# Optimization experiments

Hardware: AMD Instinct MI355X
Metric: run time of the kernel (lower is better)

## Reference

```python
import jax, jax.numpy as jnp
import numpy as np

N_NODES = 50000
N_EDGES = 600000
N_GRAPHS = 1024
D = 128
NEG_SLOPE = 0.2


def _gat_conv(x, W, a_src, a_dst, b, src, dst, n):
    # PyG GATConv, heads=1, concat=True, add_self_loops=True (self loops
    # already appended to src/dst by the caller).
    h = x @ W                                  # [N, C]
    alpha_src = h @ a_src                      # [N]
    alpha_dst = h @ a_dst                      # [N]
    e = jax.nn.leaky_relu(alpha_src[src] + alpha_dst[dst], NEG_SLOPE)  # [E']
    # segment softmax over incoming edges of each destination node
    e_max = jax.ops.segment_max(e, dst, num_segments=n)
    ex = jnp.exp(e - e_max[dst])
    denom = jax.ops.segment_sum(ex, dst, num_segments=n)
    alpha = ex / denom[dst]
    out = jax.ops.segment_sum(h[src] * alpha[:, None], dst, num_segments=n)
    return out + b


def _global_mean_pool(x, batch, n_graphs):
    s = jax.ops.segment_sum(x, batch, num_segments=n_graphs)
    cnt = jax.ops.segment_sum(jnp.ones((x.shape[0],), x.dtype), batch,
                              num_segments=n_graphs)
    return s / jnp.maximum(cnt, 1.0)[:, None]


def setup_inputs() -> dict:
    key = jax.random.key(0)
    ks = jax.random.split(key, 12)
    x = jax.random.normal(ks[0], (N_NODES, D), dtype=jnp.float32)
    edge_index = jax.random.randint(ks[1], (2, N_EDGES), 0, N_NODES, dtype=jnp.int64)
    batch = jnp.sort(jax.random.randint(ks[2], (N_NODES,), 0, N_GRAPHS, dtype=jnp.int64))
    glorot = 1.0 / np.sqrt(D)
    return {
        "x": x,
        "edge_index": edge_index,
        "batch": batch,
        "W1": jax.random.normal(ks[3], (D, D), dtype=jnp.float32) * glorot,
        "att_src1": jax.random.normal(ks[4], (D,), dtype=jnp.float32) * glorot,
        "att_dst1": jax.random.normal(ks[5], (D,), dtype=jnp.float32) * glorot,
        "b1": jnp.zeros((D,), dtype=jnp.float32),
        "W2": jax.random.normal(ks[6], (D, D), dtype=jnp.float32) * glorot,
        "att_src2": jax.random.normal(ks[7], (D,), dtype=jnp.float32) * glorot,
        "att_dst2": jax.random.normal(ks[8], (D,), dtype=jnp.float32) * glorot,
        "b2": jnp.zeros((D,), dtype=jnp.float32),
    }


def reference(x, edge_index, batch, W1, att_src1, att_dst1, b1,
              W2, att_src2, att_dst2, b2):
    n = x.shape[0]
    loops = jnp.arange(n, dtype=edge_index.dtype)
    src = jnp.concatenate([edge_index[0], loops])
    dst = jnp.concatenate([edge_index[1], loops])

    h1 = jax.nn.relu(_gat_conv(x, W1, att_src1, att_dst1, b1, src, dst, n))
    emb1 = _global_mean_pool(h1, batch, N_GRAPHS)

    h2 = jax.nn.relu(_gat_conv(h1, W2, att_src2, att_dst2, b2, src, dst, n))
    emb2 = _global_mean_pool(h2, batch, N_GRAPHS)

    return (emb1, emb2)
```

## Files before the change

### kernel.cpp

```cpp
#include <hip/hip_runtime.h>
#include <hip/hip_fp16.h>
#include <cstdint>
#include <cstddef>

#define NN 50000
#define NE 600000
#define NT (NE + NN)
#define NG 1024
#define D 128
#define NEG_SLOPE 0.2f
#define MAXDEG 64

typedef _Float16 half8 __attribute__((ext_vector_type(8)));
typedef float f32x4 __attribute__((ext_vector_type(4)));

__global__ void prep_misc(const float* __restrict__ W1, const float* __restrict__ W2,
                          _Float16* __restrict__ Wt1, _Float16* __restrict__ Wt2,
                          const int* __restrict__ batch, int* __restrict__ gptr,
                          unsigned* __restrict__ deg) {
    int i = blockIdx.x * 256 + threadIdx.x;
    if (i < NN) deg[i] = 0u;
    if (i < 2 * D * D) {
        const float* W  = (i < D * D) ? W1 : W2;
        _Float16*   Wt  = (i < D * D) ? Wt1 : Wt2;
        int j = i & (D * D - 1);
        int k = j >> 7, c = j & 127;
        Wt[c * D + k] = (_Float16)W[j];
    }
    if (i <= NG) {
        int lo = 0, hi = NN;
        while (lo < hi) { int mid = (lo + hi) >> 1; if (batch[mid] < i) lo = mid + 1; else hi = mid; }
        gptr[i] = lo;
    }
}

__global__ void build_kernel(const int* __restrict__ ei0, const int* __restrict__ ei1,
                             unsigned* __restrict__ deg,
                             unsigned short* __restrict__ bucket) {
    int e = blockIdx.x * blockDim.x + threadIdx.x;
    if (e >= NT) return;
    int s, d;
    if (e < NE) { s = ei0[e]; d = ei1[e]; } else { s = d = e - NE; }
    unsigned pos = atomicAdd(deg + d, 1u);
    if (pos < MAXDEG) bucket[(size_t)d * MAXDEG + pos] = (unsigned short)s;
}

template <bool FP16IN>
__global__ __launch_bounds__(256) void gemm_mfma(
    const void* __restrict__ Xv, const _Float16* __restrict__ Wt,
    const float* __restrict__ a_s, const float* __restrict__ a_d,
    __half2* __restrict__ Hh, float* __restrict__ AS, float* __restrict__ AD)
{
    __shared__ _Float16 Ht[64][132];
    int t = threadIdx.x;
    int w = t >> 6, lane = t & 63;
    int rowlane = lane & 15, kg = lane >> 4;
    int rb = (int)blockIdx.x * 64;
    int r0 = rb + w * 16;
    int r  = r0 + rowlane;
    int rc = r < NN ? r : NN - 1;

    half8 afr[4];
    if constexpr (FP16IN) {
        const _Float16* xr = (const _Float16*)Xv + (size_t)rc * D + kg * 8;
        #pragma unroll
        for (int kt = 0; kt < 4; ++kt)
            afr[kt] = *reinterpret_cast<const half8*>(xr + kt * 32);
    } else {
        const float* xr = (const float*)Xv + (size_t)rc * D + kg * 8;
        #pragma unroll
        for (int kt = 0; kt < 4; ++kt) {
            float4 u = *reinterpret_cast<const float4*>(xr + kt * 32);
            float4 v = *reinterpret_cast<const float4*>(xr + kt * 32 + 4);
            half8 a;
            a[0] = (_Float16)u.x; a[1] = (_Float16)u.y;
            a[2] = (_Float16)u.z; a[3] = (_Float16)u.w;
            a[4] = (_Float16)v.x; a[5] = (_Float16)v.y;
            a[6] = (_Float16)v.z; a[7] = (_Float16)v.w;
            afr[kt] = a;
        }
    }

    f32x4 acc[8];
    #pragma unroll
    for (int i = 0; i < 8; ++i) acc[i] = (f32x4){0.f, 0.f, 0.f, 0.f};

    const _Float16* wb = Wt + (size_t)rowlane * D + kg * 8;
    #pragma unroll
    for (int ct = 0; ct < 8; ++ct) {
        const _Float16* wc = wb + (size_t)ct * 16 * D;
        #pragma unroll
        for (int kt = 0; kt < 4; ++kt) {
            half8 b = *reinterpret_cast<const half8*>(wc + kt * 32);
            acc[ct] = __builtin_amdgcn_mfma_f32_16x16x32_f16(afr[kt], b, acc[ct], 0, 0, 0);
        }
    }

    float rs[4] = {0.f, 0.f, 0.f, 0.f}, rd[4] = {0.f, 0.f, 0.f, 0.f};
    #pragma unroll
    for (int ct = 0; ct < 8; ++ct) {
        float as_c = a_s[ct * 16 + rowlane];
        float ad_c = a_d[ct * 16 + rowlane];
        #pragma unroll
        for (int reg = 0; reg < 4; ++reg) {
            float v = acc[ct][reg];
            rs[reg] += v * as_c;
            rd[reg] += v * ad_c;
            Ht[w * 16 + kg * 4 + reg][ct * 16 + rowlane] = (_Float16)v;
        }
    }
    #pragma unroll
    for (int reg = 0; reg < 4; ++reg) {
        #pragma unroll
        for (int off = 1; off < 16; off <<= 1) {
            rs[reg] += __shfl_xor(rs[reg], off, 64);
            rd[reg] += __shfl_xor(rd[reg], off, 64);
        }
    }
    if (rowlane == 0) {
        #pragma unroll
        for (int reg = 0; reg < 4; ++reg) {
            int rr = r0 + kg * 4 + reg;
            if (rr < NN) { AS[rr] = rs[reg]; AD[rr] = rd[reg]; }
        }
    }
    __syncthreads();
    #pragma unroll
    for (int it = 0; it < 8; ++it) {
        int u = t + it * 256;
        int row = u >> 5, cu = u & 31;
        int g = rb + row;
        if (g < NN) {
            uint2 v = *reinterpret_cast<const uint2*>(&Ht[row][cu * 4]);
            *reinterpret_cast<uint2*>(Hh + (size_t)g * 64 + cu * 2) = v;
        }
    }
}

__device__ __forceinline__ void acc8(float w, uint4 v, float* a) {
    float2 p;
    p = __half22float2(*reinterpret_cast<const __half2*>(&v.x)); a[0] += w * p.x; a[1] += w * p.y;
    p = __half22float2(*reinterpret_cast<const __half2*>(&v.y)); a[2] += w * p.x; a[3] += w * p.y;
    p = __half22float2(*reinterpret_cast<const __half2*>(&v.z)); a[4] += w * p.x; a[5] += w * p.y;
    p = __half22float2(*reinterpret_cast<const __half2*>(&v.w)); a[6] += w * p.x; a[7] += w * p.y;
}

__global__ __launch_bounds__(256) void gat_node(
    const unsigned* __restrict__ degv, const unsigned short* __restrict__ bucket,
    const float* __restrict__ AS, const float* __restrict__ AD,
    const uint4* __restrict__ Hh, const float* __restrict__ B,
    uint4* __restrict__ HOUT)
{
    int wid  = (int)((blockIdx.x * blockDim.x + threadIdx.x) >> 6);
    int lane = threadIdx.x & 63;
    int l16  = lane & 15;
    int nid  = wid * 4 + (lane >> 4);
    if (nid >= NN) return;

    int deg = (int)degv[nid];
    if (deg > MAXDEG) deg = MAXDEG;
    int beg = nid * MAXDEG;
    float ad_d = AD[nid];

    float m = -3.0e38f, den = 0.f;
    float a[8] = {0.f, 0.f, 0.f, 0.f, 0.f, 0.f, 0.f, 0.f};
    const uint4* hb = Hh + l16;

    for (int c0 = 0; c0 < deg; c0 += 16) {
        int cnt = deg - c0; if (cnt > 16) cnt = 16;

        int   s_l = 0;
        float e_l = -3.0e38f;
        if (l16 < cnt) {
            s_l = (int)bucket[beg + c0 + l16];
            float e = AS[s_l] + ad_d;
            e_l = e > 0.f ? e : e * NEG_SLOPE;
        }
        float cm = e_l;
        #pragma unroll
        for (int off = 8; off; off >>= 1)
            cm = fmaxf(cm, __shfl_xor(cm, off, 16));
        float mn = fmaxf(m, cm);
        float w_l = (l16 < cnt) ? __expf(e_l - mn) : 0.f;
        float cs = w_l;
        #pragma unroll
        for (int off = 8; off; off >>= 1)
            cs += __shfl_xor(cs, off, 16);
        float f = __expf(m - mn);
        den = den * f + cs;
        #pragma unroll
        for (int i = 0; i < 8; ++i) a[i] *= f;
        m = mn;

        int   sj[16];
        float wj[16];
        #pragma unroll
        for (int j = 0; j < 16; ++j) {
            sj[j] = __shfl(s_l, j, 16);
            wj[j] = __shfl(w_l, j, 16);
        }
        uint4 hv[16];
        #pragma unroll
        for (int j = 0; j < 16; ++j)
            hv[j] = hb[(size_t)sj[j] * 16];
        #pragma unroll
        for (int j = 0; j < 16; ++j)
            acc8(wj[j], hv[j], a);
    }

    float inv = 1.0f / den;
    float4 b0 = *reinterpret_cast<const float4*>(B + l16 * 8);
    float4 b1 = *reinterpret_cast<const float4*>(B + l16 * 8 + 4);
    float o0 = fmaxf(a[0] * inv + b0.x, 0.f);
    float o1 = fmaxf(a[1] * inv + b0.y, 0.f);
    float o2 = fmaxf(a[2] * inv + b0.z, 0.f);
    float o3 = fmaxf(a[3] * inv + b0.w, 0.f);
    float o4 = fmaxf(a[4] * inv + b1.x, 0.f);
    float o5 = fmaxf(a[5] * inv + b1.y, 0.f);
    float o6 = fmaxf(a[6] * inv + b1.z, 0.f);
    float o7 = fmaxf(a[7] * inv + b1.w, 0.f);
    __half2 p0 = __floats2half2_rn(o0, o1);
    __half2 p1 = __floats2half2_rn(o2, o3);
    __half2 p2 = __floats2half2_rn(o4, o5);
    __half2 p3 = __floats2half2_rn(o6, o7);
    uint4 pv;
    pv.x = *reinterpret_cast<unsigned*>(&p0);
    pv.y = *reinterpret_cast<unsigned*>(&p1);
    pv.z = *reinterpret_cast<unsigned*>(&p2);
    pv.w = *reinterpret_cast<unsigned*>(&p3);
    HOUT[(size_t)nid * 16 + l16] = pv;
}

__global__ __launch_bounds__(128) void pool_kernel(
    const __half* __restrict__ houth, const int* __restrict__ gptr,
    float* __restrict__ OUT)
{
    int g = blockIdx.x, c = threadIdx.x;
    int lo = gptr[g], hi = gptr[g + 1];
    float s0 = 0.f, s1 = 0.f, s2 = 0.f, s3 = 0.f;
    int r = lo;
    for (; r + 4 <= hi; r += 4) {
        s0 += __half2float(houth[(size_t)(r + 0) * D + c]);
        s1 += __half2float(houth[(size_t)(r + 1) * D + c]);
        s2 += __half2float(houth[(size_t)(r + 2) * D + c]);
        s3 += __half2float(houth[(size_t)(r + 3) * D + c]);
    }
    for (; r < hi; ++r) s0 += __half2float(houth[(size_t)r * D + c]);
    float s = (s0 + s1) + (s2 + s3);
    float n = (float)(hi - lo);
    OUT[(size_t)g * D + c] = s / fmaxf(n, 1.f);
}

extern "C" void kernel_launch(void* const* d_in, const int* in_sizes, int n_in,
                              void* d_out, int out_size, void* d_ws, size_t ws_size,
                              hipStream_t stream)
{
    const float* x     = (const float*)d_in[0];
    const int*   ei    = (const int*)d_in[1];
    const int*   batch = (const int*)d_in[2];
    const float* W[2]    = { (const float*)d_in[3], (const float*)d_in[7] };
    const float* ASV[2]  = { (const float*)d_in[4], (const float*)d_in[8] };
    const float* ADV[2]  = { (const float*)d_in[5], (const float*)d_in[9] };
    const float* BV[2]   = { (const float*)d_in[6], (const float*)d_in[10] };
    float* out = (float*)d_out;
    float* ws  = (float*)d_ws;

    const int* ei0 = ei;
    const int* ei1 = ei + NE;

    const int NB = (NN + 255) / 256;

    size_t o = 0;
    unsigned* deg   = (unsigned*)(ws + o); o += NN;
    __half2*  Hh    = (__half2*)(ws + o);  o += (size_t)NN * 64;
    __half2*  houth = (__half2*)(ws + o);  o += (size_t)NN * 64;
    float*    asb   = ws + o;              o += NN;
    float*    adb   = ws + o;              o += NN;
    unsigned short* bucket = (unsigned short*)(ws + o); o += (size_t)NN * MAXDEG / 2;
    int*      gptr  = (int*)(ws + o);      o += NG + 1;
    _Float16* Wt1   = (_Float16*)(ws + o); o += (D * D) / 2;
    _Float16* Wt2   = (_Float16*)(ws + o); o += (D * D) / 2;

    const int edge_blocks = (NT + 255) / 256;
    const int gemm_blocks = (NN + 63) / 64;
    const int gat_blocks  = (NN / 4 + 3) / 4;

    prep_misc<<<NB, 256, 0, stream>>>(W[0], W[1], Wt1, Wt2, batch, gptr, deg);
    build_kernel<<<edge_blocks, 256, 0, stream>>>(ei0, ei1, deg, bucket);

    gemm_mfma<false><<<gemm_blocks, 256, 0, stream>>>(x, Wt1, ASV[0], ADV[0],
                                                      Hh, asb, adb);
    gat_node<<<gat_blocks, 256, 0, stream>>>(deg, bucket, asb, adb, (const uint4*)Hh,
                                             BV[0], (uint4*)houth);
    pool_kernel<<<NG, 128, 0, stream>>>((const __half*)houth, gptr, out);

    gemm_mfma<true><<<gemm_blocks, 256, 0, stream>>>(houth, Wt2, ASV[1], ADV[1],
                                                     Hh, asb, adb);
    gat_node<<<gat_blocks, 256, 0, stream>>>(deg, bucket, asb, adb, (const uint4*)Hh,
                                             BV[1], (uint4*)houth);
    pool_kernel<<<NG, 128, 0, stream>>>((const __half*)houth, gptr, out + (size_t)NG * D);
}
```

Measured before the change: 172.7 us.

## Fuse layer-2 GEMM with layer-1 pooling and process two edges per build thread

Merges the second GEMM and the first mean-pool into a single launch with disjoint block ranges, so the two independent stages overlap and one launch is saved. The build kernel now handles two edges per thread using vectorized int2 index loads. The GAT output store is made nontemporal, and the second pool runs as 256-thread blocks with half the threads idle. The nontemporal store may evict data that the following kernels reread.

```diff
diff --git a/kernel.cpp b/kernel.cpp
--- a/kernel.cpp
+++ b/kernel.cpp
@@ -11,8 +11,11 @@
 #define NEG_SLOPE 0.2f
 #define MAXDEG 64
 
+#define GEMM_BLOCKS ((NN + 63) / 64)
+
 typedef _Float16 half8 __attribute__((ext_vector_type(8)));
 typedef float f32x4 __attribute__((ext_vector_type(4)));
+typedef unsigned int u32x4 __attribute__((ext_vector_type(4)));
 
 __global__ void prep_misc(const float* __restrict__ W1, const float* __restrict__ W2,
                           _Float16* __restrict__ Wt1, _Float16* __restrict__ Wt2,
@@ -37,25 +40,34 @@
 __global__ void build_kernel(const int* __restrict__ ei0, const int* __restrict__ ei1,
                              unsigned* __restrict__ deg,
                              unsigned short* __restrict__ bucket) {
-    int e = blockIdx.x * blockDim.x + threadIdx.x;
+    int e = (blockIdx.x * blockDim.x + threadIdx.x) * 2;
     if (e >= NT) return;
-    int s, d;
-    if (e < NE) { s = ei0[e]; d = ei1[e]; } else { s = d = e - NE; }
-    unsigned pos = atomicAdd(deg + d, 1u);
-    if (pos < MAXDEG) bucket[(size_t)d * MAXDEG + pos] = (unsigned short)s;
+    int s0, d0, s1, d1;
+    if (e < NE) {
+        int2 sv = *reinterpret_cast<const int2*>(ei0 + e);
+        int2 dv = *reinterpret_cast<const int2*>(ei1 + e);
+        s0 = sv.x; d0 = dv.x; s1 = sv.y; d1 = dv.y;
+    } else {
+        s0 = d0 = e - NE;
+        s1 = d1 = e + 1 - NE;
+    }
+    unsigned p0 = atomicAdd(deg + d0, 1u);
+    if (p0 < MAXDEG) bucket[(size_t)d0 * MAXDEG + p0] = (unsigned short)s0;
+    unsigned p1 = atomicAdd(deg + d1, 1u);
+    if (p1 < MAXDEG) bucket[(size_t)d1 * MAXDEG + p1] = (unsigned short)s1;
 }
 
 template <bool FP16IN>
-__global__ __launch_bounds__(256) void gemm_mfma(
-    const void* __restrict__ Xv, const _Float16* __restrict__ Wt,
+__device__ __forceinline__ void gemm_body(
+    int bid, const void* __restrict__ Xv, const _Float16* __restrict__ Wt,
     const float* __restrict__ a_s, const float* __restrict__ a_d,
     __half2* __restrict__ Hh, float* __restrict__ AS, float* __restrict__ AD)
 {
     __shared__ _Float16 Ht[64][132];
-    int t = threadIdx.x;
+    int t = (int)threadIdx.x;
     int w = t >> 6, lane = t & 63;
     int rowlane = lane & 15, kg = lane >> 4;
-    int rb = (int)blockIdx.x * 64;
+    int rb = bid * 64;
     int r0 = rb + w * 16;
     int r  = r0 + rowlane;
     int rc = r < NN ? r : NN - 1;
@@ -135,6 +147,52 @@
             *reinterpret_cast<uint2*>(Hh + (size_t)g * 64 + cu * 2) = v;
         }
     }
+}
+
+__device__ __forceinline__ void pool_body(int g, const __half* __restrict__ houth,
+                                          const int* __restrict__ gptr,
+                                          float* __restrict__ OUT) {
+    int c = (int)threadIdx.x;
+    if (c >= 128) return;
+    int lo = gptr[g], hi = gptr[g + 1];
+    float s0 = 0.f, s1 = 0.f, s2 = 0.f, s3 = 0.f;
+    int r = lo;
+    for (; r + 4 <= hi; r += 4) {
+        s0 += __half2float(houth[(size_t)(r + 0) * D + c]);
+        s1 += __half2float(houth[(size_t)(r + 1) * D + c]);
+        s2 += __half2float(houth[(size_t)(r + 2) * D + c]);
+        s3 += __half2float(houth[(size_t)(r + 3) * D + c]);
+    }
+    for (; r < hi; ++r) s0 += __half2float(houth[(size_t)r * D + c]);
+    float s = (s0 + s1) + (s2 + s3);
+    float n = (float)(hi - lo);
+    OUT[(size_t)g * D + c] = s / fmaxf(n, 1.f);
+}
+
+__global__ __launch_bounds__(256) void gemm_mfma1(
+    const float* __restrict__ X, const _Float16* __restrict__ Wt,
+    const float* __restrict__ a_s, const float* __restrict__ a_d,
+    __half2* __restrict__ Hh, float* __restrict__ AS, float* __restrict__ AD)
+{
+    gemm_body<false>((int)blockIdx.x, X, Wt, a_s, a_d, Hh, AS, AD);
+}
+
+__global__ __launch_bounds__(256) void gemm2_pool1(
+    const void* __restrict__ houth, const _Float16* __restrict__ Wt,
+    const float* __restrict__ a_s, const float* __restrict__ a_d,
+    __half2* __restrict__ Hh, float* __restrict__ AS, float* __restrict__ AD,
+    const int* __restrict__ gptr, float* __restrict__ OUT)
+{
+    int b = (int)blockIdx.x;
+    if (b < GEMM_BLOCKS) gemm_body<true>(b, houth, Wt, a_s, a_d, Hh, AS, AD);
+    else                 pool_body(b - GEMM_BLOCKS, (const __half*)houth, gptr, OUT);
+}
+
+__global__ __launch_bounds__(256) void pool2_kernel(
+    const __half* __restrict__ houth, const int* __restrict__ gptr,
+    float* __restrict__ OUT)
+{
+    pool_body((int)blockIdx.x, houth, gptr, OUT);
 }
 
 __device__ __forceinline__ void acc8(float w, uint4 v, float* a) {
@@ -223,32 +281,12 @@
     __half2 p1 = __floats2half2_rn(o2, o3);
     __half2 p2 = __floats2half2_rn(o4, o5);
     __half2 p3 = __floats2half2_rn(o6, o7);
-    uint4 pv;
+    u32x4 pv;
     pv.x = *reinterpret_cast<unsigned*>(&p0);
     pv.y = *reinterpret_cast<unsigned*>(&p1);
     pv.z = *reinterpret_cast<unsigned*>(&p2);
     pv.w = *reinterpret_cast<unsigned*>(&p3);
-    HOUT[(size_t)nid * 16 + l16] = pv;
-}
-
-__global__ __launch_bounds__(128) void pool_kernel(
-    const __half* __restrict__ houth, const int* __restrict__ gptr,
-    float* __restrict__ OUT)
-{
-    int g = blockIdx.x, c = threadIdx.x;
-    int lo = gptr[g], hi = gptr[g + 1];
-    float s0 = 0.f, s1 = 0.f, s2 = 0.f, s3 = 0.f;
-    int r = lo;
-    for (; r + 4 <= hi; r += 4) {
-        s0 += __half2float(houth[(size_t)(r + 0) * D + c]);
-        s1 += __half2float(houth[(size_t)(r + 1) * D + c]);
-        s2 += __half2float(houth[(size_t)(r + 2) * D + c]);
-        s3 += __half2float(houth[(size_t)(r + 3) * D + c]);
-    }
-    for (; r < hi; ++r) s0 += __half2float(houth[(size_t)r * D + c]);
-    float s = (s0 + s1) + (s2 + s3);
-    float n = (float)(hi - lo);
-    OUT[(size_t)g * D + c] = s / fmaxf(n, 1.f);
+    __builtin_nontemporal_store(pv, reinterpret_cast<u32x4*>(&HOUT[(size_t)nid * 16 + l16]));
 }
 
 extern "C" void kernel_launch(void* const* d_in, const int* in_sizes, int n_in,
@@ -281,22 +319,20 @@
     _Float16* Wt1   = (_Float16*)(ws + o); o += (D * D) / 2;
     _Float16* Wt2   = (_Float16*)(ws + o); o += (D * D) / 2;
 
-    const int edge_blocks = (NT + 255) / 256;
-    const int gemm_blocks = (NN + 63) / 64;
-    const int gat_blocks  = (NN / 4 + 3) / 4;
+    const int build_blocks = (NT / 2 + 255) / 256;
+    const int gat_blocks   = (NN / 4 + 3) / 4;
 
     prep_misc<<<NB, 256, 0, stream>>>(W[0], W[1], Wt1, Wt2, batch, gptr, deg);
-    build_kernel<<<edge_blocks, 256, 0, stream>>>(ei0, ei1, deg, bucket);
-
-    gemm_mfma<false><<<gemm_blocks, 256, 0, stream>>>(x, Wt1, ASV[0], ADV[0],
-                                                      Hh, asb, adb);
+    build_kernel<<<build_blocks, 256, 0, stream>>>(ei0, ei1, deg, bucket);
+
+    gemm_mfma1<<<GEMM_BLOCKS, 256, 0, stream>>>(x, Wt1, ASV[0], ADV[0], Hh, asb, adb);
     gat_node<<<gat_blocks, 256, 0, stream>>>(deg, bucket, asb, adb, (const uint4*)Hh,
                                              BV[0], (uint4*)houth);
-    pool_kernel<<<NG, 128, 0, stream>>>((const __half*)houth, gptr, out);
-
-    gemm_mfma<true><<<gemm_blocks, 256, 0, stream>>>(houth, Wt2, ASV[1], ADV[1],
-                                                     Hh, asb, adb);
+
+    gemm2_pool1<<<GEMM_BLOCKS + NG, 256, 0, stream>>>(
+        houth, Wt2, ASV[1], ADV[1], Hh, asb, adb, gptr, out);
+
     gat_node<<<gat_blocks, 256, 0, stream>>>(deg, bucket, asb, adb, (const uint4*)Hh,
                                              BV[1], (uint4*)houth);
-    pool_kernel<<<NG, 128, 0, stream>>>((const __half*)houth, gptr, out + (size_t)NG * D);
-}
+    pool2_kernel<<<NG, 256, 0, stream>>>((const __half*)houth, gptr, out + (size_t)NG * D);
+}
```

Result: no change. 170.6 us (-1.2%).
